# Kernel tuning notes

Measured on AMD Instinct MI355X. Metric: run time of the kernel, lower is better.

Reference implementation:

```python
import jax, jax.numpy as jnp
import numpy as np

# Stream_PreNet with kernels [[1,7],[7,1]], conv2d_bn=False, conv2d_activation=None.
# SelfConv2d builds im2col patches via SYMMETRIC padding + shifted slices, then a Dense.
# That is mathematically a conv2d with 'same'-style SYMMETRIC padding, so we implement
# it as symmetric pad + VALID conv (same math, no giant im2col intermediate).

C_IN = 8
C_OUT = 96


def _selfconv2d(x, w, b, kh, kw):
    # x: [B,H,W,C], w: [kh,kw,C,F] (HWIO), b: [F]
    ph, pw = kh // 2, kw // 2
    xp = jnp.pad(x, ((0, 0), (ph, ph), (pw, pw), (0, 0)), mode='symmetric')
    out = jax.lax.conv_general_dilated(
        xp, w, window_strides=(1, 1), padding='VALID',
        dimension_numbers=('NHWC', 'HWIO', 'NHWC'))
    return out + b


def setup_inputs() -> dict:
    key = jax.random.key(0)
    k0, k1, k2, k3, k4 = jax.random.split(key, 5)
    feature_in = jax.random.normal(k0, (8, 512, 256, C_IN), dtype=jnp.float32)
    # layer 0: kernel [1,7], C_IN -> C_OUT ; layer 1: kernel [7,1], C_OUT -> C_OUT
    s1 = 1.0 / np.sqrt(1 * 7 * C_IN)
    s2 = 1.0 / np.sqrt(7 * 1 * C_OUT)
    W1 = jax.random.normal(k1, (1, 7, C_IN, C_OUT), dtype=jnp.float32) * s1
    b1 = jax.random.normal(k2, (C_OUT,), dtype=jnp.float32) * 0.01
    W2 = jax.random.normal(k3, (7, 1, C_OUT, C_OUT), dtype=jnp.float32) * s2
    b2 = jax.random.normal(k4, (C_OUT,), dtype=jnp.float32) * 0.01
    return {'feature_in': feature_in, 'W1': W1, 'b1': b1, 'W2': W2, 'b2': b2,
            'training': 0}


def reference(feature_in, W1, b1, W2, b2, training):
    # conv2d_bn=False, activation=None -> plain conv stack, training unused
    out = _selfconv2d(feature_in, W1, b1, 1, 7)   # [B,T,F,C_OUT]
    out = _selfconv2d(out, W2, b2, 7, 1)          # [B,T,F,C_OUT]
    return out
```

## Files before the change

kernel.cpp:

```cpp
#include <hip/hip_runtime.h>


#define B_   8
#define H_   512
#define W_   256
#define CIN  8
#define COUT 96
#define TH   8
#define TW   16
#define RS   (TH + 6)
#define XC   22
#define XCP  23
#define KP   416
#define NTHREADS 384

typedef __bf16 bf16x8 __attribute__((ext_vector_type(8)));
typedef float  f32x4  __attribute__((ext_vector_type(4)));
typedef int    i32x4  __attribute__((ext_vector_type(4)));

__device__ __forceinline__ unsigned short f2bf(float f) {
  unsigned u = __builtin_bit_cast(unsigned, f);
  u += 0x7FFFu + ((u >> 16) & 1u);
  return (unsigned short)(u >> 16);
}

__device__ __forceinline__ bf16x8 ld16s(const unsigned short* p) {
  i32x4 t = *(const i32x4*)p;
  return __builtin_bit_cast(bf16x8, t);
}

__device__ __forceinline__ f32x4 mfma16(bf16x8 a, bf16x8 b, f32x4 c) {
  return __builtin_amdgcn_mfma_f32_16x16x32_bf16(a, b, c, 0, 0, 0);
}

__device__ __forceinline__ int symH(int i) { return i < 0 ? -1 - i : (i >= H_ ? 2 * H_ - 1 - i : i); }
__device__ __forceinline__ int symW(int i) { return i < 0 ? -1 - i : (i >= W_ ? 2 * W_ - 1 - i : i); }

__global__ void prep_kernel(const float* __restrict__ W1, const float* __restrict__ b1,
                            const float* __restrict__ W2, const float* __restrict__ b2,
                            unsigned short* __restrict__ wct, float* __restrict__ bias2e) {
  int i = blockIdx.x * 256 + threadIdx.x;
  if (i < 96 * KP) {
    int n = i / KP, k = i - n * KP;
    int p = k >> 3, c = k & 7;
    float s = 0.f;
    if (p < 49) {
      int th = p / 7, tw = p - 7 * th;
#pragma unroll 8
      for (int m = 0; m < 96; ++m)
        s += W2[(th * 96 + m) * 96 + n] * W1[(tw * 8 + c) * 96 + m];
    }
    wct[i] = f2bf(s);
  }
  if (i < 96) {
    float s = b2[i];
#pragma unroll 8
    for (int kc = 0; kc < 672; ++kc) {
      int m = kc - (kc / 96) * 96;
      s += W2[kc * 96 + i] * b1[m];
    }
    bias2e[i] = s;
  }
}

__global__ __launch_bounds__(NTHREADS, 5)
void conv7(const float* __restrict__ x, const unsigned short* __restrict__ wct,
           const float* __restrict__ bias2e, float* __restrict__ out) {
  __shared__ __align__(16) unsigned short xt[RS][XCP][CIN];

  const int tid = threadIdx.x;
  const int w0  = blockIdx.x * TW;
  const int h0  = blockIdx.y * TH;
  const int b   = blockIdx.z;

  const int wid  = tid >> 6;
  const int lane = tid & 63;
  const int l15  = lane & 15;
  const int g    = lane >> 4;
  const int cf   = wid * 16 + l15;

  const float* xb = x + (size_t)b * H_ * W_ * CIN;
  if (tid < RS * XC) {
    int rr = tid / XC, cc = tid - rr * XC;
    int hr = symH(h0 - 3 + rr);
    int wc = symW(w0 - 3 + cc);
    const float4* px = (const float4*)(xb + ((size_t)hr * W_ + wc) * CIN);
    float4 v0 = px[0], v1 = px[1];
    unsigned p0 = ((unsigned)f2bf(v0.y) << 16) | f2bf(v0.x);
    unsigned p1 = ((unsigned)f2bf(v0.w) << 16) | f2bf(v0.z);
    unsigned p2 = ((unsigned)f2bf(v1.y) << 16) | f2bf(v1.x);
    unsigned p3 = ((unsigned)f2bf(v1.w) << 16) | f2bf(v1.z);
    *(i32x4*)&xt[rr][cc][0] = (i32x4){(int)p0, (int)p1, (int)p2, (int)p3};
  }

  const unsigned short* wrow = wct + (size_t)cf * KP;
  const i32x4 z4 = {0, 0, 0, 0};

  f32x4 acc[TH];
#pragma unroll
  for (int m = 0; m < TH; ++m) acc[m] = (f32x4){0.f, 0.f, 0.f, 0.f};

  __syncthreads();

#pragma unroll 1
  for (int pass = 0; pass < 2; ++pass) {
    if (pass == 0) {
      bf16x8 wf[7];
#pragma unroll
      for (int s = 0; s < 7; ++s) wf[s] = ld16s(&wrow[32 * s + 8 * g]);
#pragma unroll
      for (int s = 0; s < 7; ++s) {
        int p = 4 * s + g;
        int th = p / 7, tw = p - 7 * th;
        const unsigned short* bp = &xt[th][l15 + tw][0];
#pragma unroll
        for (int m = 0; m < TH; ++m)
          acc[m] = mfma16(wf[s], ld16s(bp + m * XCP * CIN), acc[m]);
      }
    } else {
      bf16x8 wf[6];
#pragma unroll
      for (int s = 0; s < 6; ++s) wf[s] = ld16s(&wrow[32 * (7 + s) + 8 * g]);
#pragma unroll
      for (int s = 0; s < 6; ++s) {
        int p = 4 * (7 + s) + g;
        int th = p / 7, tw = p - 7 * th;
        const unsigned short* bp = &xt[th][l15 + tw][0];
        if (s < 5) {
#pragma unroll
          for (int m = 0; m < TH; ++m)
            acc[m] = mfma16(wf[s], ld16s(bp + m * XCP * CIN), acc[m]);
        } else {
#pragma unroll
          for (int m = 0; m < TH; ++m) {
            bf16x8 xv = (g == 0) ? ld16s(bp + m * XCP * CIN)
                                 : __builtin_bit_cast(bf16x8, z4);
            acc[m] = mfma16(wf[s], xv, acc[m]);
          }
        }
      }
    }
  }

  const float4 bia = *(const float4*)&bias2e[wid * 16 + 4 * g];
  const size_t obase = (((size_t)b * H_ + h0) * W_ + (w0 + l15)) * COUT + wid * 16 + 4 * g;
#pragma unroll
  for (int m = 0; m < TH; ++m) {
    f32x4 v = acc[m];
    v[0] += bia.x; v[1] += bia.y; v[2] += bia.z; v[3] += bia.w;
    __builtin_nontemporal_store(v, (f32x4*)(out + obase + (size_t)m * (W_ * COUT)));
  }
}

extern "C" void kernel_launch(void* const* d_in, const int* in_sizes, int n_in,
                              void* d_out, int out_size, void* d_ws, size_t ws_size,
                              hipStream_t stream) {
  const float* x  = (const float*)d_in[0];
  const float* W1 = (const float*)d_in[1];
  const float* b1 = (const float*)d_in[2];
  const float* W2 = (const float*)d_in[3];
  const float* b2 = (const float*)d_in[4];

  unsigned short* wct = (unsigned short*)d_ws;
  float* bias2e = (float*)(wct + 96 * KP);
  float* out = (float*)d_out;

  prep_kernel<<<dim3(156), dim3(256), 0, stream>>>(W1, b1, W2, b2, wct, bias2e);
  conv7<<<dim3(W_ / TW, H_ / TH, B_), dim3(NTHREADS), 0, stream>>>(
      x, wct, bias2e, out);
}
```

Baseline: 145.7 us.

## Switch fused conv to 32x32x16 MFMA with larger 16x32 spatial tiles

Replaces the 16x16x32 bf16 MFMA with 32x32x16 MFMA, so each wave computes 32 output channels by 32 columns. Each instruction now packs two filter taps, and the padded tap count drops to 50. The spatial tile grows from 8x16 to 16x32, cutting the halo overhead of the symmetric-padded input loads. Waves are split across three channel groups and two row groups, and the LDS row padding is removed. The larger tile and accumulators reduce occupancy, and the new store pattern plus unpadded LDS rows may bring less coalesced writes or bank conflicts.

```diff
diff --git a/kernel.cpp b/kernel.cpp
--- a/kernel.cpp
+++ b/kernel.cpp
@@ -6,16 +6,16 @@
 #define W_   256
 #define CIN  8
 #define COUT 96
-#define TH   8
-#define TW   16
+#define TH   16
+#define TW   32
 #define RS   (TH + 6)
-#define XC   22
-#define XCP  23
-#define KP   416
+#define XC   (TW + 6)
+#define KP   400
 #define NTHREADS 384
 
 typedef __bf16 bf16x8 __attribute__((ext_vector_type(8)));
 typedef float  f32x4  __attribute__((ext_vector_type(4)));
+typedef float  f32x16 __attribute__((ext_vector_type(16)));
 typedef int    i32x4  __attribute__((ext_vector_type(4)));
 
 __device__ __forceinline__ unsigned short f2bf(float f) {
@@ -29,8 +29,8 @@
   return __builtin_bit_cast(bf16x8, t);
 }
 
-__device__ __forceinline__ f32x4 mfma16(bf16x8 a, bf16x8 b, f32x4 c) {
-  return __builtin_amdgcn_mfma_f32_16x16x32_bf16(a, b, c, 0, 0, 0);
+__device__ __forceinline__ f32x16 mfma32(bf16x8 a, bf16x8 b, f32x16 c) {
+  return __builtin_amdgcn_mfma_f32_32x32x16_bf16(a, b, c, 0, 0, 0);
 }
 
 __device__ __forceinline__ int symH(int i) { return i < 0 ? -1 - i : (i >= H_ ? 2 * H_ - 1 - i : i); }
@@ -63,10 +63,10 @@
   }
 }
 
-__global__ __launch_bounds__(NTHREADS, 5)
+__global__ __launch_bounds__(NTHREADS, 4)
 void conv7(const float* __restrict__ x, const unsigned short* __restrict__ wct,
            const float* __restrict__ bias2e, float* __restrict__ out) {
-  __shared__ __align__(16) unsigned short xt[RS][XCP][CIN];
+  __shared__ __align__(16) unsigned short xt[RS][XC][CIN];
 
   const int tid = threadIdx.x;
   const int w0  = blockIdx.x * TW;
@@ -75,13 +75,15 @@
 
   const int wid  = tid >> 6;
   const int lane = tid & 63;
-  const int l15  = lane & 15;
-  const int g    = lane >> 4;
-  const int cf   = wid * 16 + l15;
+  const int l31  = lane & 31;
+  const int hi   = lane >> 5;
+  const int cht  = wid >> 1;
+  const int rg   = wid & 1;
+  const int ch   = cht * 32 + l31;
 
   const float* xb = x + (size_t)b * H_ * W_ * CIN;
-  if (tid < RS * XC) {
-    int rr = tid / XC, cc = tid - rr * XC;
+  for (int idx = tid; idx < RS * XC; idx += NTHREADS) {
+    int rr = idx / XC, cc = idx - rr * XC;
     int hr = symH(h0 - 3 + rr);
     int wc = symW(w0 - 3 + cc);
     const float4* px = (const float4*)(xb + ((size_t)hr * W_ + wc) * CIN);
@@ -93,62 +95,53 @@
     *(i32x4*)&xt[rr][cc][0] = (i32x4){(int)p0, (int)p1, (int)p2, (int)p3};
   }
 
-  const unsigned short* wrow = wct + (size_t)cf * KP;
-  const i32x4 z4 = {0, 0, 0, 0};
-
-  f32x4 acc[TH];
-#pragma unroll
-  for (int m = 0; m < TH; ++m) acc[m] = (f32x4){0.f, 0.f, 0.f, 0.f};
+  const unsigned short* wrow = wct + (size_t)ch * KP;
+  const unsigned short* xtf  = &xt[0][0][0];
 
   __syncthreads();
 
+#define ROWSTR (XC * CIN)
+
 #pragma unroll 1
-  for (int pass = 0; pass < 2; ++pass) {
-    if (pass == 0) {
-      bf16x8 wf[7];
+  for (int qr = 0; qr < 2; ++qr) {
+    const int m0 = rg * 8 + qr * 4;
+    f32x16 acc0 = {}, acc1 = {}, acc2 = {}, acc3 = {};
+    const int mbase = m0 * ROWSTR + l31 * CIN;
+
+#pragma unroll 1
+    for (int sp = 0; sp < 5; ++sp) {
+      bf16x8 wf[5];
 #pragma unroll
-      for (int s = 0; s < 7; ++s) wf[s] = ld16s(&wrow[32 * s + 8 * g]);
+      for (int s2 = 0; s2 < 5; ++s2)
+        wf[s2] = ld16s(&wrow[80 * sp + 16 * s2 + 8 * hi]);
 #pragma unroll
-      for (int s = 0; s < 7; ++s) {
-        int p = 4 * s + g;
-        int th = p / 7, tw = p - 7 * th;
-        const unsigned short* bp = &xt[th][l15 + tw][0];
-#pragma unroll
-        for (int m = 0; m < TH; ++m)
-          acc[m] = mfma16(wf[s], ld16s(bp + m * XCP * CIN), acc[m]);
-      }
-    } else {
-      bf16x8 wf[6];
-#pragma unroll
-      for (int s = 0; s < 6; ++s) wf[s] = ld16s(&wrow[32 * (7 + s) + 8 * g]);
-#pragma unroll
-      for (int s = 0; s < 6; ++s) {
-        int p = 4 * (7 + s) + g;
-        int th = p / 7, tw = p - 7 * th;
-        const unsigned short* bp = &xt[th][l15 + tw][0];
-        if (s < 5) {
-#pragma unroll
-          for (int m = 0; m < TH; ++m)
-            acc[m] = mfma16(wf[s], ld16s(bp + m * XCP * CIN), acc[m]);
-        } else {
-#pragma unroll
-          for (int m = 0; m < TH; ++m) {
-            bf16x8 xv = (g == 0) ? ld16s(bp + m * XCP * CIN)
-                                 : __builtin_bit_cast(bf16x8, z4);
-            acc[m] = mfma16(wf[s], xv, acc[m]);
-          }
-        }
+      for (int s2 = 0; s2 < 5; ++s2) {
+        int p = 10 * sp + 2 * s2 + hi;
+        int pc = p > 48 ? 48 : p;
+        int th = (pc * 9363) >> 16;
+        int tw = pc - 7 * th;
+        const unsigned short* bp = xtf + mbase + th * ROWSTR + tw * CIN;
+        acc0 = mfma32(wf[s2], ld16s(bp), acc0);
+        acc1 = mfma32(wf[s2], ld16s(bp + ROWSTR), acc1);
+        acc2 = mfma32(wf[s2], ld16s(bp + 2 * ROWSTR), acc2);
+        acc3 = mfma32(wf[s2], ld16s(bp + 3 * ROWSTR), acc3);
       }
     }
-  }
 
-  const float4 bia = *(const float4*)&bias2e[wid * 16 + 4 * g];
-  const size_t obase = (((size_t)b * H_ + h0) * W_ + (w0 + l15)) * COUT + wid * 16 + 4 * g;
-#pragma unroll
-  for (int m = 0; m < TH; ++m) {
-    f32x4 v = acc[m];
-    v[0] += bia.x; v[1] += bia.y; v[2] += bia.z; v[3] += bia.w;
-    __builtin_nontemporal_store(v, (f32x4*)(out + obase + (size_t)m * (W_ * COUT)));
+#define EPI(R, ACC)                                                              \
+    {                                                                            \
+      const size_t ob = (((size_t)b * H_ + h0 + m0 + (R)) * W_ + w0 + l31) * COUT \
+                        + cht * 32 + 4 * hi;                                     \
+      _Pragma("unroll")                                                          \
+      for (int q = 0; q < 4; ++q) {                                              \
+        const float4 bia = *(const float4*)&bias2e[cht * 32 + 8 * q + 4 * hi];   \
+        f32x4 v = {(ACC)[4 * q] + bia.x, (ACC)[4 * q + 1] + bia.y,               \
+                   (ACC)[4 * q + 2] + bia.z, (ACC)[4 * q + 3] + bia.w};          \
+        __builtin_nontemporal_store(v, (f32x4*)(out + ob + 8 * q));              \
+      }                                                                          \
+    }
+    EPI(0, acc0) EPI(1, acc1) EPI(2, acc2) EPI(3, acc3)
+#undef EPI
   }
 }
 
@@ -165,7 +158,7 @@
   float* bias2e = (float*)(wct + 96 * KP);
   float* out = (float*)d_out;
 
-  prep_kernel<<<dim3(156), dim3(256), 0, stream>>>(W1, b1, W2, b2, wct, bias2e);
+  prep_kernel<<<dim3(150), dim3(256), 0, stream>>>(W1, b1, W2, b2, wct, bias2e);
   conv7<<<dim3(W_ / TW, H_ / TH, B_), dim3(NTHREADS), 0, stream>>>(
       x, wct, bias2e, out);
 }
```

Result: slower. 379.7 us (+160.5%).

## Double tile height and give each wave two channel groups to reuse input fragments

Applied to the files above, without the earlier changes.

Doubles the row tile to 16 and remaps the six waves so each one covers 32 output channels across 8 rows. Every LDS input fragment now feeds two MFMAs, which halves LDS reads per MFMA and shrinks the halo overhead relative to the tile. Weights are loaded in three smaller passes to keep register pressure manageable, and occupancy is lowered to 3 blocks. Output stores switch from nontemporal to regular stores.

```diff
diff --git a/kernel.cpp b/kernel.cpp
--- a/kernel.cpp
+++ b/kernel.cpp
@@ -6,7 +6,7 @@
 #define W_   256
 #define CIN  8
 #define COUT 96
-#define TH   8
+#define TH   16
 #define TW   16
 #define RS   (TH + 6)
 #define XC   22
@@ -63,7 +63,7 @@
   }
 }
 
-__global__ __launch_bounds__(NTHREADS, 5)
+__global__ __launch_bounds__(NTHREADS, 3)
 void conv7(const float* __restrict__ x, const unsigned short* __restrict__ wct,
            const float* __restrict__ bias2e, float* __restrict__ out) {
   __shared__ __align__(16) unsigned short xt[RS][XCP][CIN];
@@ -77,11 +77,14 @@
   const int lane = tid & 63;
   const int l15  = lane & 15;
   const int g    = lane >> 4;
-  const int cf   = wid * 16 + l15;
+  const int chg  = wid >> 1;
+  const int rg   = wid & 1;
+  const int m0   = rg * 8;
+  const int ch0  = chg * 32 + l15;
 
   const float* xb = x + (size_t)b * H_ * W_ * CIN;
-  if (tid < RS * XC) {
-    int rr = tid / XC, cc = tid - rr * XC;
+  for (int idx = tid; idx < RS * XC; idx += NTHREADS) {
+    int rr = idx / XC, cc = idx - rr * XC;
     int hr = symH(h0 - 3 + rr);
     int wc = symW(w0 - 3 + cc);
     const float4* px = (const float4*)(xb + ((size_t)hr * W_ + wc) * CIN);
@@ -93,62 +96,59 @@
     *(i32x4*)&xt[rr][cc][0] = (i32x4){(int)p0, (int)p1, (int)p2, (int)p3};
   }
 
-  const unsigned short* wrow = wct + (size_t)cf * KP;
+  const unsigned short* wrow0 = wct + (size_t)ch0 * KP;
+  const unsigned short* wrow1 = wrow0 + (size_t)16 * KP;
+  const unsigned short* xtf   = &xt[0][0][0];
   const i32x4 z4 = {0, 0, 0, 0};
 
-  f32x4 acc[TH];
+  f32x4 acc0[8], acc1[8];
 #pragma unroll
-  for (int m = 0; m < TH; ++m) acc[m] = (f32x4){0.f, 0.f, 0.f, 0.f};
+  for (int m = 0; m < 8; ++m) { acc0[m] = (f32x4){0,0,0,0}; acc1[m] = (f32x4){0,0,0,0}; }
 
   __syncthreads();
 
+#define ROWSTR (XCP * CIN)
+
+#define PASS(S0, NS, HAS_TAIL)                                                  \
+  { bf16x8 wf0[NS], wf1[NS];                                                    \
+    _Pragma("unroll") for (int s2 = 0; s2 < (NS); ++s2) {                       \
+      wf0[s2] = ld16s(&wrow0[32 * ((S0) + s2) + 8 * g]);                        \
+      wf1[s2] = ld16s(&wrow1[32 * ((S0) + s2) + 8 * g]);                        \
+    }                                                                           \
+    _Pragma("unroll") for (int s2 = 0; s2 < (NS); ++s2) {                       \
+      int p = 4 * ((S0) + s2) + g;                                              \
+      int pc = p > 48 ? 48 : p;                                                 \
+      int th = (pc * 9363) >> 16;               \
+      int tw = pc - 7 * th;                                                     \
+      const unsigned short* bp = xtf + (m0 + th) * ROWSTR + (l15 + tw) * CIN;   \
+      const bool tail = (HAS_TAIL) && ((S0) + s2 == 12) && (g != 0);            \
+      _Pragma("unroll") for (int m = 0; m < 8; ++m) {                           \
+        bf16x8 xv = tail ? __builtin_bit_cast(bf16x8, z4)                       \
+                         : ld16s(bp + m * ROWSTR);                              \
+        acc0[m] = mfma16(wf0[s2], xv, acc0[m]);                                 \
+        acc1[m] = mfma16(wf1[s2], xv, acc1[m]);                                 \
+      }                                                                         \
+    } }
+
 #pragma unroll 1
-  for (int pass = 0; pass < 2; ++pass) {
-    if (pass == 0) {
-      bf16x8 wf[7];
+  for (int pass = 0; pass < 3; ++pass) {
+    if (pass == 0)      { PASS(0, 5, 0) }
+    else if (pass == 1) { PASS(5, 4, 0) }
+    else                { PASS(9, 4, 1) }
+  }
+#undef PASS
+
+  const float4 bia0 = *(const float4*)&bias2e[chg * 32 + 4 * g];
+  const float4 bia1 = *(const float4*)&bias2e[chg * 32 + 16 + 4 * g];
+  const size_t ob0 = (((size_t)b * H_ + h0 + m0) * W_ + (w0 + l15)) * COUT + chg * 32 + 4 * g;
 #pragma unroll
-      for (int s = 0; s < 7; ++s) wf[s] = ld16s(&wrow[32 * s + 8 * g]);
-#pragma unroll
-      for (int s = 0; s < 7; ++s) {
-        int p = 4 * s + g;
-        int th = p / 7, tw = p - 7 * th;
-        const unsigned short* bp = &xt[th][l15 + tw][0];
-#pragma unroll
-        for (int m = 0; m < TH; ++m)
-          acc[m] = mfma16(wf[s], ld16s(bp + m * XCP * CIN), acc[m]);
-      }
-    } else {
-      bf16x8 wf[6];
-#pragma unroll
-      for (int s = 0; s < 6; ++s) wf[s] = ld16s(&wrow[32 * (7 + s) + 8 * g]);
-#pragma unroll
-      for (int s = 0; s < 6; ++s) {
-        int p = 4 * (7 + s) + g;
-        int th = p / 7, tw = p - 7 * th;
-        const unsigned short* bp = &xt[th][l15 + tw][0];
-        if (s < 5) {
-#pragma unroll
-          for (int m = 0; m < TH; ++m)
-            acc[m] = mfma16(wf[s], ld16s(bp + m * XCP * CIN), acc[m]);
-        } else {
-#pragma unroll
-          for (int m = 0; m < TH; ++m) {
-            bf16x8 xv = (g == 0) ? ld16s(bp + m * XCP * CIN)
-                                 : __builtin_bit_cast(bf16x8, z4);
-            acc[m] = mfma16(wf[s], xv, acc[m]);
-          }
-        }
-      }
-    }
-  }
-
-  const float4 bia = *(const float4*)&bias2e[wid * 16 + 4 * g];
-  const size_t obase = (((size_t)b * H_ + h0) * W_ + (w0 + l15)) * COUT + wid * 16 + 4 * g;
-#pragma unroll
-  for (int m = 0; m < TH; ++m) {
-    f32x4 v = acc[m];
-    v[0] += bia.x; v[1] += bia.y; v[2] += bia.z; v[3] += bia.w;
-    __builtin_nontemporal_store(v, (f32x4*)(out + obase + (size_t)m * (W_ * COUT)));
+  for (int m = 0; m < 8; ++m) {
+    f32x4 v0 = acc0[m], v1 = acc1[m];
+    v0[0] += bia0.x; v0[1] += bia0.y; v0[2] += bia0.z; v0[3] += bia0.w;
+    v1[0] += bia1.x; v1[1] += bia1.y; v1[2] += bia1.z; v1[3] += bia1.w;
+    const size_t ob = ob0 + (size_t)m * (W_ * COUT);
+    *(f32x4*)(out + ob)      = v0;
+    *(f32x4*)(out + ob + 16) = v1;
   }
 }
 
```

Result: slower. 262.9 us (+80.4%).
